# Optimization experiments

Measured on AMD Instinct MI355X. Metric: run time of the kernel, lower is better.

The kernel has to match this reference:

```python
import jax, jax.numpy as jnp
import numpy as np

B, MAX_OBJS, D = 8, 12, 512
NUM_OBJ, NUM_ACT, NUM_TRS = 37, 6, 3
EMBED = 128
NUM_AA = 100
NUM_CLASSES = 300
ACT_THRES = 0.5
K = MAX_OBJS * NUM_ACT            # 72 candidate (object, action) slots
FINAL_DIM = 2 * (D + 2 * EMBED)   # 1536
# All ordered pairs (i, j), i != j, in lexicographic order. itertools.permutations
# over a sorted index subset is exactly the valid-masked subsequence of this list.
_pairs = np.array([(i, j) for i in range(K) for j in range(K) if i != j], dtype=np.int64)
PAIR_I = jnp.asarray(_pairs[:, 0])
PAIR_J = jnp.asarray(_pairs[:, 1])
P = _pairs.shape[0]               # K*(K-1) = 5112 (static max num pairs)


def setup_inputs() -> dict:
    key = jax.random.key(0)
    ks = jax.random.split(key, 12)
    inp = jax.random.normal(ks[0], (B, MAX_OBJS, D), jnp.float32)
    objmask = jnp.ones((B, MAX_OBJS), jnp.float32)
    # -1 marks 'no composite-action target' for that (obj, act) slot
    AAidxs_tgts = jax.random.randint(ks[1], (B, K), -1, NUM_AA)
    TR_tgts = jax.random.uniform(ks[2], (B, K, K, NUM_TRS), jnp.float32)
    obj_act_lookup = jax.random.randint(ks[3], (NUM_OBJ, NUM_ACT), 0, NUM_AA)
    aa_aa_tr_lookup = jax.random.randint(ks[4], (NUM_AA, NUM_AA, NUM_TRS), 0, NUM_CLASSES)
    s = lambda k, shape: (jax.random.normal(k, shape, jnp.float32) * 0.02)
    return {
        'inp': inp, 'objmask': objmask,
        'TR_tgts': TR_tgts,
        'W_obj': s(ks[5], (NUM_OBJ, D)), 'b_obj': jnp.zeros((NUM_OBJ,), jnp.float32),
        'W_act': s(ks[6], (NUM_ACT, D)), 'b_act': jnp.zeros((NUM_ACT,), jnp.float32),
        'W_tr': s(ks[7], (NUM_TRS, FINAL_DIM)), 'b_tr': jnp.zeros((NUM_TRS,), jnp.float32),
        'W_ne': s(ks[8], (NUM_CLASSES, D)), 'b_ne': jnp.zeros((NUM_CLASSES,), jnp.float32),
        'obj_emb': s(ks[9], (NUM_OBJ, EMBED)), 'act_emb': s(ks[10], (NUM_ACT, EMBED)),
        'AAidxs_tgts': AAidxs_tgts,
        'obj_act_lookup': obj_act_lookup,
        'aa_aa_tr_lookup': aa_aa_tr_lookup,
    }


def reference(inp, objmask, TR_tgts, W_obj, b_obj, W_act, b_act, W_tr, b_tr,
              W_ne, b_ne, obj_emb, act_emb, AAidxs_tgts, obj_act_lookup,
              aa_aa_tr_lookup):
    # training branch (is_eval=False); obj_act_lookup only used in eval branch
    exp_objmask = jnp.repeat(objmask, NUM_ACT, axis=1)                # [B,K]
    masked = inp * objmask[:, :, None]
    pooled = masked.sum(axis=1) / objmask.sum(axis=1, keepdims=True)  # [B,D]
    non_exist_out = pooled @ W_ne.T + b_ne                            # [B,C]
    obj_out = inp @ W_obj.T + b_obj                                   # [B,MO,NO]
    act_out = inp @ W_act.T + b_act                                   # [B,MO,NA]

    posb_action_idxs = jnp.tile(jnp.arange(NUM_ACT), (B, MAX_OBJS))   # [B,K]
    pred_obj_idxs = jnp.repeat(jnp.argmax(obj_out, axis=-1), NUM_ACT, axis=1)  # [B,K]
    posb_inputs = jnp.repeat(inp, NUM_ACT, axis=1)                    # [B,K,D]

    pred_act = (jax.nn.sigmoid(act_out.reshape(B, K)) > ACT_THRES).astype(jnp.float32)
    pred_act = pred_act * exp_objmask
    selected = (pred_act == 1.0) & (AAidxs_tgts != -1)                # [B,K]
    aaidx = jnp.where(selected, AAidxs_tgts, -1)

    posb_obj_emb = obj_emb[pred_obj_idxs]                             # [B,K,E]
    posb_act_emb = act_emb[posb_action_idxs]                          # [B,K,E]
    comp = jnp.concatenate([posb_inputs, posb_obj_emb, posb_act_emb], axis=-1)  # [B,K,FINAL/2]

    # pack valid pairs to the front (stable sort preserves lexicographic order,
    # matching itertools.permutations over the sorted selected index set)
    valid = selected[:, PAIR_I] & selected[:, PAIR_J]                 # [B,P]
    order = jnp.argsort(~valid, axis=1, stable=True)                  # [B,P]
    valid_p = jnp.take_along_axis(valid, order, axis=1)
    i_p = jnp.take_along_axis(jnp.broadcast_to(PAIR_I, (B, P)), order, axis=1)
    j_p = jnp.take_along_axis(jnp.broadcast_to(PAIR_J, (B, P)), order, axis=1)
    b_ix = jnp.arange(B)[:, None]

    pair_out = jnp.where(valid_p[..., None],
                         jnp.concatenate([comp[b_ix, i_p], comp[b_ix, j_p]], axis=-1),
                         -1.0)                                        # [B,P,FINAL_DIM]
    pair_logits = pair_out @ W_tr.T + b_tr                            # [B,P,3]

    aai = aaidx[b_ix, i_p]
    aaj = aaidx[b_ix, j_p]
    ca = aa_aa_tr_lookup[jnp.maximum(aai, 0), jnp.maximum(aaj, 0)]    # [B,P,3]
    ca = jnp.where(valid_p[..., None], ca, -1)
    tr_targets = jnp.where(valid_p[..., None], TR_tgts[b_ix, i_p, j_p], -1.0)

    # diag(logit) @ one_hot(ca) then masked max over pairs == segment max per class
    flat_logit = pair_logits.reshape(B, P * NUM_TRS)
    flat_ca = ca.reshape(B, P * NUM_TRS)
    flat_valid = jnp.repeat(valid_p, NUM_TRS, axis=1)
    seg = jnp.where(flat_valid, flat_ca, NUM_CLASSES)                 # dump invalid to extra segment
    seg_max = jax.vmap(lambda l, s: jax.ops.segment_max(l, s, num_segments=NUM_CLASSES + 1))(
        flat_logit, seg)[:, :NUM_CLASSES]                             # [B,C]
    counts = jax.vmap(lambda s: jax.ops.segment_sum(jnp.ones_like(s), s, num_segments=NUM_CLASSES + 1))(
        seg)[:, :NUM_CLASSES]
    exist = counts > 0
    final_outputs = jnp.where(exist, seg_max, non_exist_out)          # [B,C]

    return final_outputs, pair_logits, tr_targets, act_out, obj_out
```

## Files before the change

kernel.cpp:

```cpp
#include <hip/hip_runtime.h>
#include <hip/hip_bf16.h>

#define Bn    8
#define MO    12
#define Dd    512
#define NOBJ  37
#define NACT  6
#define NTRS  3
#define EMB   128
#define NAA   100
#define NCLS  300
#define Kk    72
#define Pp    5112
#define HALF  768
#define FD    1536

#define OUT_FINAL 0
#define OUT_PLOG  (Bn*NCLS)
#define OUT_TTGT  (OUT_PLOG + Bn*Pp*NTRS)
#define OUT_ACT   (OUT_TTGT + Bn*Pp*NTRS)
#define OUT_OBJ   (OUT_ACT + Bn*Kk)

#define WS_LINP 0
#define WS_EO   (WS_LINP + Bn*MO*6)
#define WS_EA   (WS_EO + NOBJ*6)
#define WS_INV  (WS_EA + NACT*6)
#define WS_NE   840
#define WS_OBJ  (WS_NE + Bn*NCLS)
#define WS_ACT  (WS_OBJ + Bn*MO*NOBJ)

__device__ __forceinline__ unsigned fmap(float f) {
  unsigned u = __float_as_uint(f);
  return (u & 0x80000000u) ? ~u : (u | 0x80000000u);
}
__device__ __forceinline__ float funmap(unsigned u) {
  return __uint_as_float((u & 0x80000000u) ? (u & 0x7fffffffu) : ~u);
}

__device__ __forceinline__ float wreduce(float v) {
#pragma unroll
  for (int off = 32; off > 0; off >>= 1) v += __shfl_xor(v, off, 64);
  return v;
}

__device__ __forceinline__ float dotW(const float* __restrict__ wrow,
                                      float4 x0, float4 x1, int lane) {
  const float4* w4 = (const float4*)wrow;
  float4 w0 = w4[lane], w1 = w4[lane + 64];
  float s0 = fmaf(w0.x, x0.x, fmaf(w0.y, x0.y, fmaf(w0.z, x0.z, w0.w * x0.w)));
  float s1 = fmaf(w1.x, x1.x, fmaf(w1.y, x1.y, fmaf(w1.z, x1.z, w1.w * x1.w)));
  return wreduce(s0 + s1);
}

__device__ __forceinline__ float dot512_wave(const float* __restrict__ a,
                                             const float* __restrict__ b, int lane) {
  const float4* b4 = (const float4*)b;
  return dotW(a, b4[lane], b4[lane + 64], lane);
}

__device__ __forceinline__ float dot128_wave(const float* __restrict__ a,
                                             const float* __restrict__ b, int lane) {
  const float2* a2 = (const float2*)a;
  const float2* b2 = (const float2*)b;
  float2 x = a2[lane], y = b2[lane];
  return wreduce(fmaf(x.x, y.x, x.y * y.y));
}

#define W_OBJ_E  (Bn*MO*NOBJ)
#define W_ACT_E  (W_OBJ_E + Bn*Kk)
#define W_LINP_E (W_ACT_E + Bn*MO*6)
#define W_EO_E   (W_LINP_E + NOBJ*6)
#define W_EA_E   (W_EO_E + NACT*6)
#define W_INV_E  (W_EA_E + NTRS)
#define W_TOT    (W_INV_E + Bn*NCLS)

__global__ __launch_bounds__(256) void k1(
    const float* __restrict__ inp, const float* __restrict__ objmask,
    const float* __restrict__ W_obj, const float* __restrict__ b_obj,
    const float* __restrict__ W_act, const float* __restrict__ b_act,
    const float* __restrict__ W_tr, const float* __restrict__ b_tr,
    const float* __restrict__ W_ne, const float* __restrict__ b_ne,
    const float* __restrict__ obj_emb, const float* __restrict__ act_emb,
    float* __restrict__ out, float* __restrict__ ws)
{
  int gt = blockIdx.x * 256 + threadIdx.x;
  int w = gt >> 6, lane = gt & 63;

  if (w < W_OBJ_E) {
    int b = w / (MO*NOBJ), r = w % (MO*NOBJ), o = r / NOBJ, c = r % NOBJ;
    float v = dot512_wave(W_obj + c*Dd, inp + (b*MO + o)*Dd, lane) + b_obj[c];
    if (!lane) { out[OUT_OBJ + (b*MO + o)*NOBJ + c] = v; ws[WS_OBJ + (b*MO + o)*NOBJ + c] = v; }
  } else if (w < W_ACT_E) {
    int r = w - W_OBJ_E, b = r / Kk, k = r % Kk, o = k / NACT, a = k % NACT;
    float v = dot512_wave(W_act + a*Dd, inp + (b*MO + o)*Dd, lane) + b_act[a];
    if (!lane) { out[OUT_ACT + b*Kk + k] = v; ws[WS_ACT + b*Kk + k] = v; }
  } else if (w < W_LINP_E) {
    int r = w - W_ACT_E, b = r / (MO*6), r2 = r % (MO*6), o = r2 / 6, th = r2 % 6;
    int t = th >> 1, h = th & 1;
    float v = dot512_wave(W_tr + t*FD + h*HALF, inp + (b*MO + o)*Dd, lane);
    if (!lane) ws[WS_LINP + (b*MO + o)*6 + th] = v;
  } else if (w < W_EO_E) {
    int r = w - W_LINP_E, oc = r / 6, th = r % 6, t = th >> 1, h = th & 1;
    float v = dot128_wave(W_tr + t*FD + h*HALF + Dd, obj_emb + oc*EMB, lane);
    if (!lane) ws[WS_EO + oc*6 + th] = v;
  } else if (w < W_INV_E) {
    if (w < W_EA_E) {
      int r = w - W_EO_E, a = r / 6, th = r % 6, t = th >> 1, h = th & 1;
      float v = dot128_wave(W_tr + t*FD + h*HALF + Dd + EMB, act_emb + a*EMB, lane);
      if (!lane) ws[WS_EA + a*6 + th] = v;
    } else {
      int t = w - W_EA_E;
      const float4* w4 = (const float4*)(W_tr + t*FD);
      float s = 0.f;
#pragma unroll
      for (int i = 0; i < 6; ++i) { float4 x = w4[lane + 64*i]; s += x.x + x.y + x.z + x.w; }
      s = wreduce(s);
      if (!lane) ws[WS_INV + t] = b_tr[t] - s;
    }
  } else if (w < W_TOT) {
    int r = w - W_INV_E, b = r / NCLS, c = r % NCLS;
    const float4* i4 = (const float4*)inp;
    float msum = 0.f;
    float4 p0 = make_float4(0.f, 0.f, 0.f, 0.f), p1 = p0;
#pragma unroll
    for (int o = 0; o < MO; ++o) {
      float m = objmask[b*MO + o];
      msum += m;
      float4 v0 = i4[(b*MO + o)*128 + lane];
      float4 v1 = i4[(b*MO + o)*128 + lane + 64];
      p0.x = fmaf(m, v0.x, p0.x); p0.y = fmaf(m, v0.y, p0.y);
      p0.z = fmaf(m, v0.z, p0.z); p0.w = fmaf(m, v0.w, p0.w);
      p1.x = fmaf(m, v1.x, p1.x); p1.y = fmaf(m, v1.y, p1.y);
      p1.z = fmaf(m, v1.z, p1.z); p1.w = fmaf(m, v1.w, p1.w);
    }
    float v = dotW(W_ne + c*Dd, p0, p1, lane) / msum + b_ne[c];
    if (!lane) ws[WS_NE + b*NCLS + c] = v;
  }
}

#define NSLICE 20

__global__ __launch_bounds__(256) void k2(
    const float* __restrict__ objmask, const float* __restrict__ TRt,
    const float* __restrict__ b_tr, const int* __restrict__ AA,
    const int* __restrict__ aalut,
    float* __restrict__ out, float* __restrict__ ws)
{
  __shared__ float s_L[Kk*6];
  __shared__ float s_inv[NTRS];
  __shared__ unsigned s_seg[NCLS];
  __shared__ int s_sel[Kk], s_aa[Kk], s_C[Kk], s_vlist[Kk], s_pred[MO], s_T;

  int b = blockIdx.x / (NSLICE + 1), slice = blockIdx.x % (NSLICE + 1);
  int tid = threadIdx.x;

  if (tid < MO) {
    const float* p = ws + WS_OBJ + (b*MO + tid)*NOBJ;
    float best = p[0]; int bi = 0;
#pragma unroll
    for (int c = 1; c < NOBJ; ++c) { float v = p[c]; if (v > best) { best = v; bi = c; } }
    s_pred[tid] = bi;
  } else if (tid >= 64 && tid < 64 + Kk) {
    int k = tid - 64, o = k / NACT;
    int aa = AA[b*Kk + k];
    int sel = (ws[WS_ACT + b*Kk + k] > 0.f) && (objmask[b*MO + o] == 1.0f) && (aa != -1);
    s_sel[k] = sel;
    s_aa[k] = sel ? aa : -1;
  } else if (tid >= 192 && tid < 192 + NTRS) {
    s_inv[tid - 192] = ws[WS_INV + (tid - 192)];
  }
  __syncthreads();
  for (int m = tid; m < Kk*6; m += 256) {
    int k = m / 6, th = m % 6, t = th >> 1, h = th & 1;
    int o = k / NACT, a = k % NACT;
    float v = ws[WS_LINP + (b*MO + o)*6 + th] + ws[WS_EO + s_pred[o]*6 + th]
            + ws[WS_EA + a*6 + th];
    if (h == 0) v += b_tr[t];
    s_L[m] = v;
  }
  if (tid == 0) {
    int c = 0;
    for (int k = 0; k < Kk; ++k) { s_C[k] = c; c += s_sel[k]; }
    s_T = c;
  }
  __syncthreads();

  int T = s_T, Vtot = T*(T-1);

  if (slice < NSLICE) {
    int q = slice*256 + tid;
    if (q < Pp) {
      float* plog = out + OUT_PLOG + (size_t)b*Pp*NTRS;
      float* ttgt = out + OUT_TTGT + (size_t)b*Pp*NTRS;
      int i = q / (Kk-1);
      int jj = q - i*(Kk-1);
      int j = jj + (jj >= i ? 1 : 0);
      int si = s_sel[i], sj = s_sel[j];
      int vb = s_C[i]*(T-1) + (si ? (s_C[j] - (i < j ? 1 : 0)) : 0);
      bool valid = si && sj;
      int pos = valid ? vb : (Vtot + q - vb);
      float l0, l1, l2;
      if (valid) {
        l0 = s_L[i*6+0] + s_L[j*6+1];
        l1 = s_L[i*6+2] + s_L[j*6+3];
        l2 = s_L[i*6+4] + s_L[j*6+5];
      } else { l0 = s_inv[0]; l1 = s_inv[1]; l2 = s_inv[2]; }
      int ob = pos*3;
      plog[ob+0] = l0; plog[ob+1] = l1; plog[ob+2] = l2;
      if (valid) {
        const float* tr = TRt + (((size_t)b*Kk + i)*Kk + j)*NTRS;
        ttgt[ob+0] = tr[0]; ttgt[ob+1] = tr[1]; ttgt[ob+2] = tr[2];
      } else {
        ttgt[ob+0] = -1.f; ttgt[ob+1] = -1.f; ttgt[ob+2] = -1.f;
      }
    }
  } else {
    if (tid < Kk && s_sel[tid]) s_vlist[s_C[tid]] = tid;
    for (int c = tid; c < NCLS; c += 256) s_seg[c] = 0u;
    __syncthreads();
    for (int m = tid; m < Vtot; m += 256) {
      int vi = m / (T-1);
      int r = m - vi*(T-1);
      int vj = r + (r >= vi ? 1 : 0);
      int i = s_vlist[vi], j = s_vlist[vj];
      float l0 = s_L[i*6+0] + s_L[j*6+1];
      float l1 = s_L[i*6+2] + s_L[j*6+3];
      float l2 = s_L[i*6+4] + s_L[j*6+5];
      int base = (s_aa[i]*NAA + s_aa[j])*NTRS;
      atomicMax(&s_seg[aalut[base+0]], fmap(l0));
      atomicMax(&s_seg[aalut[base+1]], fmap(l1));
      atomicMax(&s_seg[aalut[base+2]], fmap(l2));
    }
    __syncthreads();
    for (int c = tid; c < NCLS; c += 256) {
      unsigned u = s_seg[c];
      out[OUT_FINAL + b*NCLS + c] = u ? funmap(u) : ws[WS_NE + b*NCLS + c];
    }
  }
}

extern "C" void kernel_launch(void* const* d_in, const int* in_sizes, int n_in,
                              void* d_out, int out_size, void* d_ws, size_t ws_size,
                              hipStream_t stream) {
  (void)in_sizes; (void)n_in; (void)ws_size; (void)out_size;
  const float* inp      = (const float*)d_in[0];
  const float* objmask  = (const float*)d_in[1];
  const float* TRt      = (const float*)d_in[2];
  const float* W_obj    = (const float*)d_in[3];
  const float* b_obj    = (const float*)d_in[4];
  const float* W_act    = (const float*)d_in[5];
  const float* b_act    = (const float*)d_in[6];
  const float* W_tr     = (const float*)d_in[7];
  const float* b_tr     = (const float*)d_in[8];
  const float* W_ne     = (const float*)d_in[9];
  const float* b_ne     = (const float*)d_in[10];
  const float* obj_emb  = (const float*)d_in[11];
  const float* act_emb  = (const float*)d_in[12];
  const int*   AA       = (const int*)d_in[13];
  const int*   aalut    = (const int*)d_in[15];
  float* out = (float*)d_out;
  float* ws  = (float*)d_ws;

  hipLaunchKernelGGL(k1, dim3((W_TOT + 3) / 4), dim3(256), 0, stream,
                     inp, objmask, W_obj, b_obj, W_act, b_act, W_tr, b_tr,
                     W_ne, b_ne, obj_emb, act_emb, out, ws);
  hipLaunchKernelGGL(k2, dim3(Bn * (NSLICE + 1)), dim3(256), 0, stream,
                     objmask, TRt, b_tr, AA, aalut, out, ws);
}
```

Baseline: 95.65 us.

## Fuse both kernels into one cooperative kernel and compute non-exist logits lazily

Merges the projection kernel and the pair/segment-max kernel into a single cooperative launch, separated by a grid-wide sync, to remove one launch and the inter-kernel gap. The non-exist head is no longer computed for every class up front. Each batch's final block now pools the input and evaluates W_ne only for classes that received no pair. This can skip most of the 2400 wave dot products, at the cost of a grid barrier and serial work concentrated in 8 blocks. If many classes are missing, the tail block becomes longer.

```diff
diff --git a/kernel.cpp b/kernel.cpp
--- a/kernel.cpp
+++ b/kernel.cpp
@@ -1,5 +1,8 @@
 #include <hip/hip_runtime.h>
 #include <hip/hip_bf16.h>
+#include <hip/hip_cooperative_groups.h>
+
+namespace cg = cooperative_groups;
 
 #define Bn    8
 #define MO    12
@@ -25,9 +28,16 @@
 #define WS_EO   (WS_LINP + Bn*MO*6)
 #define WS_EA   (WS_EO + NOBJ*6)
 #define WS_INV  (WS_EA + NACT*6)
-#define WS_NE   840
-#define WS_OBJ  (WS_NE + Bn*NCLS)
-#define WS_ACT  (WS_OBJ + Bn*MO*NOBJ)
+
+#define T_OBJ  (Bn*MO*NOBJ)
+#define T_ACT  (T_OBJ + Bn*Kk)
+#define T_LINP (T_ACT + Bn*MO*6)
+#define T_EO   (T_LINP + NOBJ*6)
+#define T_EA   (T_EO + NACT*6)
+#define T_INV  (T_EA + NTRS)
+
+#define GRID   256
+#define NSLICE 20
 
 __device__ __forceinline__ unsigned fmap(float f) {
   unsigned u = __float_as_uint(f);
@@ -66,96 +76,72 @@
   return wreduce(fmaf(x.x, y.x, x.y * y.y));
 }
 
-#define W_OBJ_E  (Bn*MO*NOBJ)
-#define W_ACT_E  (W_OBJ_E + Bn*Kk)
-#define W_LINP_E (W_ACT_E + Bn*MO*6)
-#define W_EO_E   (W_LINP_E + NOBJ*6)
-#define W_EA_E   (W_EO_E + NACT*6)
-#define W_INV_E  (W_EA_E + NTRS)
-#define W_TOT    (W_INV_E + Bn*NCLS)
-
-__global__ __launch_bounds__(256) void k1(
+__global__ __launch_bounds__(256) void fused(
     const float* __restrict__ inp, const float* __restrict__ objmask,
+    const float* __restrict__ TRt,
     const float* __restrict__ W_obj, const float* __restrict__ b_obj,
     const float* __restrict__ W_act, const float* __restrict__ b_act,
     const float* __restrict__ W_tr, const float* __restrict__ b_tr,
     const float* __restrict__ W_ne, const float* __restrict__ b_ne,
     const float* __restrict__ obj_emb, const float* __restrict__ act_emb,
-    float* __restrict__ out, float* __restrict__ ws)
-{
-  int gt = blockIdx.x * 256 + threadIdx.x;
-  int w = gt >> 6, lane = gt & 63;
-
-  if (w < W_OBJ_E) {
-    int b = w / (MO*NOBJ), r = w % (MO*NOBJ), o = r / NOBJ, c = r % NOBJ;
-    float v = dot512_wave(W_obj + c*Dd, inp + (b*MO + o)*Dd, lane) + b_obj[c];
-    if (!lane) { out[OUT_OBJ + (b*MO + o)*NOBJ + c] = v; ws[WS_OBJ + (b*MO + o)*NOBJ + c] = v; }
-  } else if (w < W_ACT_E) {
-    int r = w - W_OBJ_E, b = r / Kk, k = r % Kk, o = k / NACT, a = k % NACT;
-    float v = dot512_wave(W_act + a*Dd, inp + (b*MO + o)*Dd, lane) + b_act[a];
-    if (!lane) { out[OUT_ACT + b*Kk + k] = v; ws[WS_ACT + b*Kk + k] = v; }
-  } else if (w < W_LINP_E) {
-    int r = w - W_ACT_E, b = r / (MO*6), r2 = r % (MO*6), o = r2 / 6, th = r2 % 6;
-    int t = th >> 1, h = th & 1;
-    float v = dot512_wave(W_tr + t*FD + h*HALF, inp + (b*MO + o)*Dd, lane);
-    if (!lane) ws[WS_LINP + (b*MO + o)*6 + th] = v;
-  } else if (w < W_EO_E) {
-    int r = w - W_LINP_E, oc = r / 6, th = r % 6, t = th >> 1, h = th & 1;
-    float v = dot128_wave(W_tr + t*FD + h*HALF + Dd, obj_emb + oc*EMB, lane);
-    if (!lane) ws[WS_EO + oc*6 + th] = v;
-  } else if (w < W_INV_E) {
-    if (w < W_EA_E) {
-      int r = w - W_EO_E, a = r / 6, th = r % 6, t = th >> 1, h = th & 1;
-      float v = dot128_wave(W_tr + t*FD + h*HALF + Dd + EMB, act_emb + a*EMB, lane);
-      if (!lane) ws[WS_EA + a*6 + th] = v;
-    } else {
-      int t = w - W_EA_E;
-      const float4* w4 = (const float4*)(W_tr + t*FD);
-      float s = 0.f;
-#pragma unroll
-      for (int i = 0; i < 6; ++i) { float4 x = w4[lane + 64*i]; s += x.x + x.y + x.z + x.w; }
-      s = wreduce(s);
-      if (!lane) ws[WS_INV + t] = b_tr[t] - s;
-    }
-  } else if (w < W_TOT) {
-    int r = w - W_INV_E, b = r / NCLS, c = r % NCLS;
-    const float4* i4 = (const float4*)inp;
-    float msum = 0.f;
-    float4 p0 = make_float4(0.f, 0.f, 0.f, 0.f), p1 = p0;
-#pragma unroll
-    for (int o = 0; o < MO; ++o) {
-      float m = objmask[b*MO + o];
-      msum += m;
-      float4 v0 = i4[(b*MO + o)*128 + lane];
-      float4 v1 = i4[(b*MO + o)*128 + lane + 64];
-      p0.x = fmaf(m, v0.x, p0.x); p0.y = fmaf(m, v0.y, p0.y);
-      p0.z = fmaf(m, v0.z, p0.z); p0.w = fmaf(m, v0.w, p0.w);
-      p1.x = fmaf(m, v1.x, p1.x); p1.y = fmaf(m, v1.y, p1.y);
-      p1.z = fmaf(m, v1.z, p1.z); p1.w = fmaf(m, v1.w, p1.w);
-    }
-    float v = dotW(W_ne + c*Dd, p0, p1, lane) / msum + b_ne[c];
-    if (!lane) ws[WS_NE + b*NCLS + c] = v;
-  }
-}
-
-#define NSLICE 20
-
-__global__ __launch_bounds__(256) void k2(
-    const float* __restrict__ objmask, const float* __restrict__ TRt,
-    const float* __restrict__ b_tr, const int* __restrict__ AA,
-    const int* __restrict__ aalut,
+    const int* __restrict__ AA, const int* __restrict__ aalut,
     float* __restrict__ out, float* __restrict__ ws)
 {
   __shared__ float s_L[Kk*6];
   __shared__ float s_inv[NTRS];
   __shared__ unsigned s_seg[NCLS];
   __shared__ int s_sel[Kk], s_aa[Kk], s_C[Kk], s_vlist[Kk], s_pred[MO], s_T;
-
-  int b = blockIdx.x / (NSLICE + 1), slice = blockIdx.x % (NSLICE + 1);
-  int tid = threadIdx.x;
+  __shared__ int s_miss[NCLS], s_nmiss;
+  __shared__ __align__(16) float s_pool[Dd];
+
+  const int tid = threadIdx.x;
+  const int lane = tid & 63;
+
+  {
+    int gw = (blockIdx.x * 256 + tid) >> 6;
+    for (int w = gw; w < T_INV; w += GRID * 4) {
+      if (w < T_OBJ) {
+        int b = w / (MO*NOBJ), r = w % (MO*NOBJ), o = r / NOBJ, c = r % NOBJ;
+        float v = dot512_wave(W_obj + c*Dd, inp + (b*MO + o)*Dd, lane) + b_obj[c];
+        if (!lane) out[OUT_OBJ + (b*MO + o)*NOBJ + c] = v;
+      } else if (w < T_ACT) {
+        int r = w - T_OBJ, b = r / Kk, k = r % Kk, o = k / NACT, a = k % NACT;
+        float v = dot512_wave(W_act + a*Dd, inp + (b*MO + o)*Dd, lane) + b_act[a];
+        if (!lane) out[OUT_ACT + b*Kk + k] = v;
+      } else if (w < T_LINP) {
+        int r = w - T_ACT, b = r / (MO*6), r2 = r % (MO*6), o = r2 / 6, th = r2 % 6;
+        int t = th >> 1, h = th & 1;
+        float v = dot512_wave(W_tr + t*FD + h*HALF, inp + (b*MO + o)*Dd, lane);
+        if (!lane) ws[WS_LINP + (b*MO + o)*6 + th] = v;
+      } else if (w < T_EO) {
+        int r = w - T_LINP, oc = r / 6, th = r % 6, t = th >> 1, h = th & 1;
+        float v = dot128_wave(W_tr + t*FD + h*HALF + Dd, obj_emb + oc*EMB, lane);
+        if (!lane) ws[WS_EO + oc*6 + th] = v;
+      } else if (w < T_EA) {
+        int r = w - T_EO, a = r / 6, th = r % 6, t = th >> 1, h = th & 1;
+        float v = dot128_wave(W_tr + t*FD + h*HALF + Dd + EMB, act_emb + a*EMB, lane);
+        if (!lane) ws[WS_EA + a*6 + th] = v;
+      } else {
+        int t = w - T_EA;
+        const float4* w4 = (const float4*)(W_tr + t*FD);
+        float s = 0.f;
+#pragma unroll
+        for (int i = 0; i < 6; ++i) { float4 x = w4[lane + 64*i]; s += x.x + x.y + x.z + x.w; }
+        s = wreduce(s);
+        if (!lane) ws[WS_INV + t] = b_tr[t] - s;
+      }
+    }
+  }
+
+  __threadfence();
+  cg::this_grid().sync();
+
+  int bid = blockIdx.x;
+  if (bid >= Bn * (NSLICE + 1)) return;
+  int b = bid / (NSLICE + 1), slice = bid % (NSLICE + 1);
 
   if (tid < MO) {
-    const float* p = ws + WS_OBJ + (b*MO + tid)*NOBJ;
+    const float* p = out + OUT_OBJ + (b*MO + tid)*NOBJ;
     float best = p[0]; int bi = 0;
 #pragma unroll
     for (int c = 1; c < NOBJ; ++c) { float v = p[c]; if (v > best) { best = v; bi = c; } }
@@ -163,7 +149,7 @@
   } else if (tid >= 64 && tid < 64 + Kk) {
     int k = tid - 64, o = k / NACT;
     int aa = AA[b*Kk + k];
-    int sel = (ws[WS_ACT + b*Kk + k] > 0.f) && (objmask[b*MO + o] == 1.0f) && (aa != -1);
+    int sel = (out[OUT_ACT + b*Kk + k] > 0.f) && (objmask[b*MO + o] == 1.0f) && (aa != -1);
     s_sel[k] = sel;
     s_aa[k] = sel ? aa : -1;
   } else if (tid >= 192 && tid < 192 + NTRS) {
@@ -182,6 +168,7 @@
     int c = 0;
     for (int k = 0; k < Kk; ++k) { s_C[k] = c; c += s_sel[k]; }
     s_T = c;
+    s_nmiss = 0;
   }
   __syncthreads();
 
@@ -234,7 +221,31 @@
     __syncthreads();
     for (int c = tid; c < NCLS; c += 256) {
       unsigned u = s_seg[c];
-      out[OUT_FINAL + b*NCLS + c] = u ? funmap(u) : ws[WS_NE + b*NCLS + c];
+      if (u) out[OUT_FINAL + b*NCLS + c] = funmap(u);
+      else s_miss[atomicAdd(&s_nmiss, 1)] = c;
+    }
+    __syncthreads();
+    int nm = s_nmiss;
+    if (nm) {
+      float msum = 0.f;
+#pragma unroll
+      for (int o = 0; o < MO; ++o) msum += objmask[b*MO + o];
+      for (int d = tid; d < Dd; d += 256) {
+        float acc = 0.f;
+#pragma unroll
+        for (int o = 0; o < MO; ++o)
+          acc = fmaf(objmask[b*MO + o], inp[(b*MO + o)*Dd + d], acc);
+        s_pool[d] = acc / msum;
+      }
+      __syncthreads();
+      const float4* p4 = (const float4*)s_pool;
+      float4 x0 = p4[lane], x1 = p4[lane + 64];
+      int wv = tid >> 6;
+      for (int m2 = wv; m2 < nm; m2 += 4) {
+        int c = s_miss[m2];
+        float v = dotW(W_ne + c*Dd, x0, x1, lane) + b_ne[c];
+        if (!lane) out[OUT_FINAL + b*NCLS + c] = v;
+      }
     }
   }
 }
@@ -261,9 +272,13 @@
   float* out = (float*)d_out;
   float* ws  = (float*)d_ws;
 
-  hipLaunchKernelGGL(k1, dim3((W_TOT + 3) / 4), dim3(256), 0, stream,
-                     inp, objmask, W_obj, b_obj, W_act, b_act, W_tr, b_tr,
-                     W_ne, b_ne, obj_emb, act_emb, out, ws);
-  hipLaunchKernelGGL(k2, dim3(Bn * (NSLICE + 1)), dim3(256), 0, stream,
-                     objmask, TRt, b_tr, AA, aalut, out, ws);
-}
+  void* args[] = {
+    (void*)&inp, (void*)&objmask, (void*)&TRt,
+    (void*)&W_obj, (void*)&b_obj, (void*)&W_act, (void*)&b_act,
+    (void*)&W_tr, (void*)&b_tr, (void*)&W_ne, (void*)&b_ne,
+    (void*)&obj_emb, (void*)&act_emb, (void*)&AA, (void*)&aalut,
+    (void*)&out, (void*)&ws
+  };
+  hipLaunchCooperativeKernel((const void*)fused, dim3(GRID), dim3(256),
+                             args, 0, stream);
+}
```

New measurement: 154.0 us. 61.1% more time.

## Compute non-exist fallback lazily only for classes with no valid pair

Applied to the files above, without the earlier changes.

Moves the non-exist linear head (mean-pooled input times W_ne) out of the first kernel and into the segment-max block of the second kernel. There it runs only for classes that received no pair logit, gathered into a shared-memory list. The obj and act logits are now read back from the output buffer instead of duplicated workspace copies. This removes 2400 waves of mostly wasted dot products from k1. In exchange, the final per-batch block gets a serial tail of pooling plus up to 300 dot products over only 4 waves.

```diff
diff --git a/kernel.cpp b/kernel.cpp
--- a/kernel.cpp
+++ b/kernel.cpp
@@ -25,9 +25,6 @@
 #define WS_EO   (WS_LINP + Bn*MO*6)
 #define WS_EA   (WS_EO + NOBJ*6)
 #define WS_INV  (WS_EA + NACT*6)
-#define WS_NE   840
-#define WS_OBJ  (WS_NE + Bn*NCLS)
-#define WS_ACT  (WS_OBJ + Bn*MO*NOBJ)
 
 __device__ __forceinline__ unsigned fmap(float f) {
   unsigned u = __float_as_uint(f);
@@ -71,15 +68,13 @@
 #define W_LINP_E (W_ACT_E + Bn*MO*6)
 #define W_EO_E   (W_LINP_E + NOBJ*6)
 #define W_EA_E   (W_EO_E + NACT*6)
-#define W_INV_E  (W_EA_E + NTRS)
-#define W_TOT    (W_INV_E + Bn*NCLS)
+#define W_TOT    (W_EA_E + NTRS)
 
 __global__ __launch_bounds__(256) void k1(
-    const float* __restrict__ inp, const float* __restrict__ objmask,
+    const float* __restrict__ inp,
     const float* __restrict__ W_obj, const float* __restrict__ b_obj,
     const float* __restrict__ W_act, const float* __restrict__ b_act,
     const float* __restrict__ W_tr, const float* __restrict__ b_tr,
-    const float* __restrict__ W_ne, const float* __restrict__ b_ne,
     const float* __restrict__ obj_emb, const float* __restrict__ act_emb,
     float* __restrict__ out, float* __restrict__ ws)
 {
@@ -89,11 +84,11 @@
   if (w < W_OBJ_E) {
     int b = w / (MO*NOBJ), r = w % (MO*NOBJ), o = r / NOBJ, c = r % NOBJ;
     float v = dot512_wave(W_obj + c*Dd, inp + (b*MO + o)*Dd, lane) + b_obj[c];
-    if (!lane) { out[OUT_OBJ + (b*MO + o)*NOBJ + c] = v; ws[WS_OBJ + (b*MO + o)*NOBJ + c] = v; }
+    if (!lane) out[OUT_OBJ + (b*MO + o)*NOBJ + c] = v;
   } else if (w < W_ACT_E) {
     int r = w - W_OBJ_E, b = r / Kk, k = r % Kk, o = k / NACT, a = k % NACT;
     float v = dot512_wave(W_act + a*Dd, inp + (b*MO + o)*Dd, lane) + b_act[a];
-    if (!lane) { out[OUT_ACT + b*Kk + k] = v; ws[WS_ACT + b*Kk + k] = v; }
+    if (!lane) out[OUT_ACT + b*Kk + k] = v;
   } else if (w < W_LINP_E) {
     int r = w - W_ACT_E, b = r / (MO*6), r2 = r % (MO*6), o = r2 / 6, th = r2 % 6;
     int t = th >> 1, h = th & 1;
@@ -103,7 +98,7 @@
     int r = w - W_LINP_E, oc = r / 6, th = r % 6, t = th >> 1, h = th & 1;
     float v = dot128_wave(W_tr + t*FD + h*HALF + Dd, obj_emb + oc*EMB, lane);
     if (!lane) ws[WS_EO + oc*6 + th] = v;
-  } else if (w < W_INV_E) {
+  } else if (w < W_TOT) {
     if (w < W_EA_E) {
       int r = w - W_EO_E, a = r / 6, th = r % 6, t = th >> 1, h = th & 1;
       float v = dot128_wave(W_tr + t*FD + h*HALF + Dd + EMB, act_emb + a*EMB, lane);
@@ -117,45 +112,30 @@
       s = wreduce(s);
       if (!lane) ws[WS_INV + t] = b_tr[t] - s;
     }
-  } else if (w < W_TOT) {
-    int r = w - W_INV_E, b = r / NCLS, c = r % NCLS;
-    const float4* i4 = (const float4*)inp;
-    float msum = 0.f;
-    float4 p0 = make_float4(0.f, 0.f, 0.f, 0.f), p1 = p0;
-#pragma unroll
-    for (int o = 0; o < MO; ++o) {
-      float m = objmask[b*MO + o];
-      msum += m;
-      float4 v0 = i4[(b*MO + o)*128 + lane];
-      float4 v1 = i4[(b*MO + o)*128 + lane + 64];
-      p0.x = fmaf(m, v0.x, p0.x); p0.y = fmaf(m, v0.y, p0.y);
-      p0.z = fmaf(m, v0.z, p0.z); p0.w = fmaf(m, v0.w, p0.w);
-      p1.x = fmaf(m, v1.x, p1.x); p1.y = fmaf(m, v1.y, p1.y);
-      p1.z = fmaf(m, v1.z, p1.z); p1.w = fmaf(m, v1.w, p1.w);
-    }
-    float v = dotW(W_ne + c*Dd, p0, p1, lane) / msum + b_ne[c];
-    if (!lane) ws[WS_NE + b*NCLS + c] = v;
   }
 }
 
 #define NSLICE 20
 
 __global__ __launch_bounds__(256) void k2(
-    const float* __restrict__ objmask, const float* __restrict__ TRt,
-    const float* __restrict__ b_tr, const int* __restrict__ AA,
-    const int* __restrict__ aalut,
+    const float* __restrict__ inp, const float* __restrict__ objmask,
+    const float* __restrict__ TRt, const float* __restrict__ b_tr,
+    const float* __restrict__ W_ne, const float* __restrict__ b_ne,
+    const int* __restrict__ AA, const int* __restrict__ aalut,
     float* __restrict__ out, float* __restrict__ ws)
 {
   __shared__ float s_L[Kk*6];
   __shared__ float s_inv[NTRS];
   __shared__ unsigned s_seg[NCLS];
   __shared__ int s_sel[Kk], s_aa[Kk], s_C[Kk], s_vlist[Kk], s_pred[MO], s_T;
+  __shared__ int s_miss[NCLS], s_nmiss;
+  __shared__ __align__(16) float s_pool[Dd];
 
   int b = blockIdx.x / (NSLICE + 1), slice = blockIdx.x % (NSLICE + 1);
-  int tid = threadIdx.x;
+  int tid = threadIdx.x, lane = tid & 63;
 
   if (tid < MO) {
-    const float* p = ws + WS_OBJ + (b*MO + tid)*NOBJ;
+    const float* p = out + OUT_OBJ + (b*MO + tid)*NOBJ;
     float best = p[0]; int bi = 0;
 #pragma unroll
     for (int c = 1; c < NOBJ; ++c) { float v = p[c]; if (v > best) { best = v; bi = c; } }
@@ -163,7 +143,7 @@
   } else if (tid >= 64 && tid < 64 + Kk) {
     int k = tid - 64, o = k / NACT;
     int aa = AA[b*Kk + k];
-    int sel = (ws[WS_ACT + b*Kk + k] > 0.f) && (objmask[b*MO + o] == 1.0f) && (aa != -1);
+    int sel = (out[OUT_ACT + b*Kk + k] > 0.f) && (objmask[b*MO + o] == 1.0f) && (aa != -1);
     s_sel[k] = sel;
     s_aa[k] = sel ? aa : -1;
   } else if (tid >= 192 && tid < 192 + NTRS) {
@@ -182,6 +162,7 @@
     int c = 0;
     for (int k = 0; k < Kk; ++k) { s_C[k] = c; c += s_sel[k]; }
     s_T = c;
+    s_nmiss = 0;
   }
   __syncthreads();
 
@@ -234,7 +215,31 @@
     __syncthreads();
     for (int c = tid; c < NCLS; c += 256) {
       unsigned u = s_seg[c];
-      out[OUT_FINAL + b*NCLS + c] = u ? funmap(u) : ws[WS_NE + b*NCLS + c];
+      if (u) out[OUT_FINAL + b*NCLS + c] = funmap(u);
+      else s_miss[atomicAdd(&s_nmiss, 1)] = c;
+    }
+    __syncthreads();
+    int nm = s_nmiss;
+    if (nm) {
+      float msum = 0.f;
+#pragma unroll
+      for (int o = 0; o < MO; ++o) msum += objmask[b*MO + o];
+      for (int d = tid; d < Dd; d += 256) {
+        float acc = 0.f;
+#pragma unroll
+        for (int o = 0; o < MO; ++o)
+          acc = fmaf(objmask[b*MO + o], inp[(b*MO + o)*Dd + d], acc);
+        s_pool[d] = acc / msum;
+      }
+      __syncthreads();
+      const float4* p4 = (const float4*)s_pool;
+      float4 x0 = p4[lane], x1 = p4[lane + 64];
+      int wv = tid >> 6;
+      for (int m2 = wv; m2 < nm; m2 += 4) {
+        int c = s_miss[m2];
+        float v = dotW(W_ne + c*Dd, x0, x1, lane) + b_ne[c];
+        if (!lane) out[OUT_FINAL + b*NCLS + c] = v;
+      }
     }
   }
 }
@@ -262,8 +267,8 @@
   float* ws  = (float*)d_ws;
 
   hipLaunchKernelGGL(k1, dim3((W_TOT + 3) / 4), dim3(256), 0, stream,
-                     inp, objmask, W_obj, b_obj, W_act, b_act, W_tr, b_tr,
-                     W_ne, b_ne, obj_emb, act_emb, out, ws);
+                     inp, W_obj, b_obj, W_act, b_act, W_tr, b_tr,
+                     obj_emb, act_emb, out, ws);
   hipLaunchKernelGGL(k2, dim3(Bn * (NSLICE + 1)), dim3(256), 0, stream,
-                     objmask, TRt, b_tr, AA, aalut, out, ws);
-}
+                     inp, objmask, TRt, b_tr, W_ne, b_ne, AA, aalut, out, ws);
+}
```

After: 91.77 us, median of 2. 4.0% less time.
